# Kernel tuning notes

Hardware: AMD Instinct MI355X
Metric: run time of the kernel (lower is better)

## Reference

```python
import jax, jax.numpy as jnp
import numpy as np

N_CLASS = 50257
EMB = 1024
HID = 1024
BATCH = 1024  # must equal HID due to the module's [H,H] zero state init
SEQ = 128


def setup_inputs() -> dict:
    key = jax.random.key(0)
    ks = jax.random.split(key, 8)
    s_e = 1.0 / np.sqrt(EMB)
    s_h = 1.0 / np.sqrt(HID)
    X = jax.random.randint(ks[0], (BATCH, SEQ), 0, N_CLASS, dtype=jnp.int32)
    C = jax.random.normal(ks[1], (N_CLASS, EMB), dtype=jnp.float32)
    # gate order along last axis: i, f, g, o (each block of size HID)
    Wx = jax.random.uniform(ks[2], (EMB, 4 * HID), jnp.float32, -s_e, s_e)
    bx = jax.random.uniform(ks[3], (4 * HID,), jnp.float32, -s_e, s_e)
    Wh = jax.random.uniform(ks[4], (HID, 4 * HID), jnp.float32, -s_h, s_h)
    bh = jax.random.uniform(ks[5], (4 * HID,), jnp.float32, -s_h, s_h)
    W_out = jax.random.uniform(ks[6], (HID, N_CLASS), jnp.float32, -s_h, s_h)
    b_out = jnp.ones((N_CLASS,), dtype=jnp.float32)  # nn.Parameter(torch.ones)
    return {"X": X, "C": C, "Wx": Wx, "bx": bx, "Wh": Wh, "bh": bh,
            "W_out": W_out, "b_out": b_out}


def _lstm_last_hidden(xs, Wx, bx, Wh, bh):
    # xs: [S, B, E]; with zero-initialized h/c of shape [H,H] and B == H,
    # the original broadcast-buggy code reduces to a standard LSTM.
    x_proj = jnp.einsum('sbe,eg->sbg', xs, Wx) + bx  # [S, B, 4H]
    B = xs.shape[1]
    H = Wh.shape[0]
    h0 = jnp.zeros((B, H), dtype=xs.dtype)
    c0 = jnp.zeros((B, H), dtype=xs.dtype)

    def step(carry, xp):
        h, c = carry
        gates = xp + h @ Wh + bh  # [B, 4H]
        i, f, g, o = jnp.split(gates, 4, axis=-1)
        i = jax.nn.sigmoid(i)
        f = jax.nn.sigmoid(f)
        g = jnp.tanh(g)
        o = jax.nn.sigmoid(o)
        c = f * c + i * g
        h = o * jnp.tanh(c)
        return (h, c), None

    (h, _), _ = jax.lax.scan(step, (h0, c0), x_proj)
    return h  # [B, H] last timestep hidden


def reference(X, C, Wx, bx, Wh, bh, W_out, b_out):
    emb = C[X]                      # [B, S, E]
    xs = jnp.swapaxes(emb, 0, 1)    # [S, B, E]  (transpose(0,1))
    h_last = _lstm_last_hidden(xs, Wx, bx, Wh, bh)
    return h_last @ W_out + b_out   # [B, n_class]
```

## Files before the change

kernel.cpp:

```cpp
#include <hip/hip_runtime.h>
#include <hip/hip_bf16.h>

#define SEQ_   128
#define NCLS_  50257
#define EMB_   1024
#define HID_   1024
#define BATCH_ 1024
#define G4_    4096

typedef __attribute__((ext_vector_type(8))) short short8;
typedef __attribute__((ext_vector_type(4))) float f32x4;

__device__ __forceinline__ void async_copy16(void* lds, const void* g) {
  __builtin_amdgcn_global_load_lds(
      (const __attribute__((address_space(1))) void*)g,
      (__attribute__((address_space(3))) void*)lds, 16, 0, 0);
}

__device__ __forceinline__ void mfma_acc(f32x4& c, const short8& a, const short8& b) {
  asm("v_mfma_f32_16x16x32_bf16 %0, %1, %2, %0" : "+v"(c) : "v"(a), "v"(b));
}

__device__ __forceinline__ float sigmoidf_(float x) {
  return 1.f / (1.f + __expf(-x));
}
__device__ __forceinline__ float tanhf_(float x) {
  x = fminf(12.f, fmaxf(-12.f, x));
  float e = __expf(2.f * x);
  return (e - 1.f) / (e + 1.f);
}
__device__ __forceinline__ float bf2f_(ushort u) {
  return __uint_as_float(((unsigned int)u) << 16);
}

template <int EPI>
__global__ __launch_bounds__(256) void gemm_bt(
    const __hip_bfloat16* __restrict__ A, const __hip_bfloat16* __restrict__ Bt,
    float* __restrict__ outF, __hip_bfloat16* __restrict__ outB,
    int Mreal, int Nreal, int K, long ostride,
    const float* __restrict__ bias0) {
  __shared__ __align__(16) char smem[65536];

  const int tid = threadIdx.x;
  const int lane = tid & 63;
  const int w = tid >> 6;
  const int wm = w >> 1;
  const int wn = w & 1;
  const int m0 = blockIdx.y * 128;
  const int n0 = blockIdx.x * 128;

  const int fr = lane & 15;
  const int kb = (lane >> 4) * 16;
  const int swz = (fr & 7) << 4;

  f32x4 acc[4][4];
#pragma unroll
  for (int i = 0; i < 4; ++i)
#pragma unroll
    for (int j = 0; j < 4; ++j) acc[i][j] = (f32x4)(0.0f);

  auto STAGE = [&](int kc, int b) {
#pragma unroll
    for (int q = 0; q < 8; ++q) {
      const int ridx = (q & 3) * 256 + tid;
      const int row = ridx >> 3;
      const int ch = ridx & 7;
      const __hip_bfloat16* src;
      char* dst;
      if (q < 4) {
        long ar = m0 + row; if (ar >= Mreal) ar = Mreal - 1;
        src = A + ar * (long)K + kc * 64 + ch * 8;
        dst = smem + b * 16384 + ridx * 16;
      } else {
        long br = n0 + row; if (br >= Nreal) br = Nreal - 1;
        src = Bt + br * (long)K + kc * 64 + ch * 8;
        dst = smem + 32768 + b * 16384 + ridx * 16;
      }
      async_copy16(dst, src);
    }
  };

  const int KC = K >> 6;
  STAGE(0, 0);
  for (int kc = 0; kc < KC; ++kc) {
    const int b = kc & 1;
    if (kc + 1 < KC) {
      STAGE(kc + 1, b ^ 1);
      asm volatile("s_waitcnt vmcnt(8)" ::: "memory");
    } else {
      asm volatile("s_waitcnt vmcnt(0)" ::: "memory");
    }
    __builtin_amdgcn_s_barrier();
    __builtin_amdgcn_sched_barrier(0);

    short8 aR[2][4], bR[2][4];
#pragma unroll
    for (int kk = 0; kk < 2; ++kk)
#pragma unroll
      for (int f = 0; f < 4; ++f) {
        aR[kk][f] = *(const short8*)(smem + b * 16384 +
                     (wm * 64 + f * 16 + fr) * 128 + ((kk * 64 + kb) ^ swz));
        bR[kk][f] = *(const short8*)(smem + 32768 + b * 16384 +
                     (wn * 64 + f * 16 + fr) * 128 + ((kk * 64 + kb) ^ swz));
      }
#pragma unroll
    for (int fm = 0; fm < 4; ++fm)
#pragma unroll
      for (int fn = 0; fn < 4; ++fn) {
        mfma_acc(acc[fm][fn], aR[0][fm], bR[0][fn]);
        mfma_acc(acc[fm][fn], aR[1][fm], bR[1][fn]);
      }
    __builtin_amdgcn_sched_barrier(0);
    __builtin_amdgcn_s_barrier();
  }

  const int cn = lane & 15;
  const int rb = (lane >> 4) * 4;
#pragma unroll
  for (int fn = 0; fn < 4; ++fn) {
    const int col = n0 + wn * 64 + fn * 16 + cn;
    const float badd = (col < Nreal) ? bias0[col] : 0.f;
#pragma unroll
    for (int fm = 0; fm < 4; ++fm) {
#pragma unroll
      for (int r = 0; r < 4; ++r) {
        const int row = m0 + wm * 64 + fm * 16 + rb + r;
        const float v = acc[fm][fn][r] + badd;
        if (EPI == 0) {
          if (row < Mreal) outB[(long)row * ostride + col] = __float2bfloat16(v);
        } else {
          if (col < Nreal && row < Mreal) outF[(long)row * ostride + col] = v;
        }
      }
    }
  }
}

__global__ __launch_bounds__(256) void pack_b(const float* __restrict__ Wh,
                                              __hip_bfloat16* __restrict__ Bpk) {
  const int gtid = blockIdx.x * 256 + threadIdx.x;
  const int l = gtid & 63;
  const int tile = gtid >> 6;
  const int g = tile & 3;
  const int kk = (tile >> 2) & 1;
  const int kc = (tile >> 3) & 7;
  const int kh = (tile >> 6) & 1;
  const int wn = (tile >> 7) & 1;
  const int ht = tile >> 8;
  const int h = ht * 32 + wn * 16 + (l & 15);
  const int k0 = kh * 512 + kc * 64 + kk * 32 + (l >> 4) * 8;
  short8 v;
#pragma unroll
  for (int e = 0; e < 8; ++e) {
    const __hip_bfloat16 b = __float2bfloat16(Wh[(size_t)(k0 + e) * G4_ + g * 1024 + h]);
    v[e] = *reinterpret_cast<const short*>(&b);
  }
  *(short8*)(Bpk + (size_t)gtid * 8) = v;
}

__global__ __launch_bounds__(512, 2) void lstm_step(
    const __hip_bfloat16* __restrict__ hprev,
    const __hip_bfloat16* __restrict__ Bpk,
    const __hip_bfloat16* __restrict__ Epr,
    const int* __restrict__ X,
    float* __restrict__ cbuf,
    __hip_bfloat16* __restrict__ hnext,
    __hip_bfloat16* __restrict__ hfin,
    int t, int last) {
  extern __shared__ __align__(16) char smem[];
  float* gacc = (float*)smem;

  const int tid = threadIdx.x;
  const int lane = tid & 63;
  const int w = tid >> 6;
  const int wm = (w >> 1) & 1;
  const int wn = w & 1;
  const int kh = w >> 2;
  const int bid = blockIdx.x;
  const int xcd = bid & 7;
  const int j = bid >> 3;
  const int ht = xcd * 4 + (j & 3);
  const int mt = j >> 2;
  const int m0 = mt * 128;
  const int h0 = ht * 32;

  const int fr = lane & 15;
  const int kb = (lane >> 4) * 16;
  const int swz = (fr & 7) << 4;
  const int cn = lane & 15;
  const int rb = (lane >> 4) * 4;

  const int crow = tid >> 2;
  const int hq = tid & 3;
  const int prow = m0 + crow;
  const int tok1 = X[prow * SEQ_ + t];

  const __hip_bfloat16* bb =
      Bpk + (size_t)(((ht * 2 + wn) * 2 + kh) * 64) * 512 + lane * 8;

  f32x4 acc[4][4];
#pragma unroll
  for (int i = 0; i < 4; ++i)
#pragma unroll
    for (int g = 0; g < 4; ++g) acc[i][g] = (f32x4)(0.0f);

  auto STAGE_A = [&](int kc, int b) {
#pragma unroll
    for (int q = 0; q < 4; ++q) {
      const int region = q >> 1;
      const int r = (q & 1) * 512 + tid;
      const int row = r >> 3, ch = r & 7;
      const __hip_bfloat16* src =
          hprev + (size_t)(m0 + row) * HID_ + region * 512 + kc * 64 + ch * 8;
      async_copy16(smem + b * 32768 + region * 16384 + r * 16, src);
    }
  };

  short8 bR[2][2][4];

  STAGE_A(0, 0);
#pragma unroll
  for (int kk = 0; kk < 2; ++kk)
#pragma unroll
    for (int g = 0; g < 4; ++g)
      bR[0][kk][g] = *(const short8*)(bb + (0 * 8 + kk * 4 + g) * 512);
  STAGE_A(1, 1);

#pragma unroll
  for (int kc = 0; kc < 8; ++kc) {
    __builtin_amdgcn_s_barrier();
    if (kc + 1 < 8) {
#pragma unroll
      for (int kk = 0; kk < 2; ++kk)
#pragma unroll
        for (int g = 0; g < 4; ++g)
          bR[(kc + 1) & 1][kk][g] =
              *(const short8*)(bb + ((kc + 1) * 8 + kk * 4 + g) * 512);
    }
    if (kc + 2 < 8) STAGE_A(kc + 2, (kc + 2) % 3);
    if (kc < 6)      asm volatile("s_waitcnt vmcnt(24)" ::: "memory");
    else if (kc == 6) asm volatile("s_waitcnt vmcnt(20)" ::: "memory");
    else             asm volatile("s_waitcnt vmcnt(8)" ::: "memory");
    __builtin_amdgcn_sched_barrier(0);

    const char* baseA = smem + (kc % 3) * 32768 + kh * 16384;
    short8 aR[2][4];
#pragma unroll
    for (int kk = 0; kk < 2; ++kk)
#pragma unroll
      for (int f = 0; f < 4; ++f)
        aR[kk][f] = *(const short8*)(baseA + (wm * 64 + f * 16 + fr) * 128 +
                                     ((kk * 64 + kb) ^ swz));
    __builtin_amdgcn_s_setprio(1);
#pragma unroll
    for (int fm = 0; fm < 4; ++fm)
#pragma unroll
      for (int g = 0; g < 4; ++g) {
        mfma_acc(acc[fm][g], aR[0][fm], bR[kc & 1][0][g]);
        mfma_acc(acc[fm][g], aR[1][fm], bR[kc & 1][1][g]);
      }
    __builtin_amdgcn_s_setprio(0);
  }

  ushort4 ep[8];
  float cold[8];
#pragma unroll
  for (int jj = 0; jj < 8; ++jj) {
    ep[jj] = *(const ushort4*)(Epr + (size_t)tok1 * G4_ + (h0 + hq * 8 + jj) * 4);
    cold[jj] = cbuf[(size_t)prow * HID_ + h0 + hq * 8 + jj];
  }

  __syncthreads();
  if (kh == 0) {
#pragma unroll
    for (int fm = 0; fm < 4; ++fm)
#pragma unroll
      for (int g = 0; g < 4; ++g)
#pragma unroll
        for (int r = 0; r < 4; ++r)
          gacc[(wm * 64 + fm * 16 + rb + r) * 132 + (wn * 16 + cn) * 4 + g] =
              acc[fm][g][r];
  }
  __syncthreads();
  if (kh == 1) {
#pragma unroll
    for (int fm = 0; fm < 4; ++fm)
#pragma unroll
      for (int g = 0; g < 4; ++g)
#pragma unroll
        for (int r = 0; r < 4; ++r)
          gacc[(wm * 64 + fm * 16 + rb + r) * 132 + (wn * 16 + cn) * 4 + g] +=
              acc[fm][g][r];
  }
  __syncthreads();

  const float* gr = gacc + crow * 132 + hq * 32;
  f32x4 cnew0, cnew1;
  short8 hv;
#pragma unroll
  for (int jj = 0; jj < 8; ++jj) {
    const f32x4 g4 = *(const f32x4*)(gr + jj * 4);
    const float iv = sigmoidf_(g4[0] + bf2f_(ep[jj].x));
    const float fv = sigmoidf_(g4[1] + bf2f_(ep[jj].y));
    const float gv = tanhf_(g4[2] + bf2f_(ep[jj].z));
    const float ov = sigmoidf_(g4[3] + bf2f_(ep[jj].w));
    const float cv = fv * cold[jj] + iv * gv;
    if (jj < 4) cnew0[jj] = cv; else cnew1[jj - 4] = cv;
    const float hval = ov * tanhf_(cv);
    const __hip_bfloat16 hb = __float2bfloat16(hval);
    hv[jj] = *reinterpret_cast<const short*>(&hb);
  }
  float* cdst = cbuf + (size_t)prow * HID_ + h0 + hq * 8;
  *(f32x4*)cdst = cnew0;
  *(f32x4*)(cdst + 4) = cnew1;
  const int hcolb = h0 + hq * 8;
  const int hswb = (hcolb & ~63) | ((hcolb & 63) ^ ((prow & 7) << 3));
  *(short8*)(hnext + (size_t)prow * HID_ + hswb) = hv;
  if (last) *(short8*)(hfin + (size_t)prow * HID_ + hswb) = hv;
}

template <bool SWZ>
__global__ __launch_bounds__(256) void conv_bf16_k(const float* __restrict__ in,
                                                   __hip_bfloat16* __restrict__ out, int n4) {
  const int i = blockIdx.x * 256 + threadIdx.x;
  if (i >= n4) return;
  const float4 v = ((const float4*)in)[i];
  int o = i * 4;
  if (SWZ) {
    const int row = o >> 10, col = o & 1023;
    const int cs = (col & ~63) | ((col & 63) ^ ((row & 7) << 3));
    o = (o & ~1023) | cs;
  }
  out[o + 0] = __float2bfloat16(v.x);
  out[o + 1] = __float2bfloat16(v.y);
  out[o + 2] = __float2bfloat16(v.z);
  out[o + 3] = __float2bfloat16(v.w);
}

template <bool PERM, bool SWZ>
__global__ __launch_bounds__(256) void transpose_conv(const float* __restrict__ in,
                                                      __hip_bfloat16* __restrict__ out,
                                                      int R, int C) {
  __shared__ float tile[32][33];
  const int c0 = blockIdx.x * 32, r0 = blockIdx.y * 32;
  const int tx = threadIdx.x, ty = threadIdx.y;
#pragma unroll
  for (int i = 0; i < 4; ++i) {
    const int r = r0 + ty + i * 8, cc = c0 + tx;
    tile[ty + i * 8][tx] = (r < R && cc < C) ? in[(size_t)r * C + cc] : 0.f;
  }
  __syncthreads();
#pragma unroll
  for (int i = 0; i < 4; ++i) {
    const int ro = c0 + ty + i * 8, co = r0 + tx;
    if (ro < C && co < R) {
      const int n = PERM ? ((ro & 1023) * 4 + (ro >> 10)) : ro;
      int k = co;
      if (SWZ) k = (k & ~63) | ((k & 63) ^ ((n & 7) << 3));
      out[(size_t)n * R + k] = __float2bfloat16(tile[tx][ty + i * 8]);
    }
  }
}

__global__ __launch_bounds__(256) void bias_perm(const float* __restrict__ bx,
                                                 const float* __restrict__ bh,
                                                 float* __restrict__ bP) {
  const int n = blockIdx.x * 256 + threadIdx.x;
  if (n >= G4_) return;
  const int h = n >> 2, g = n & 3;
  bP[n] = bx[g * HID_ + h] + bh[g * HID_ + h];
}

extern "C" void kernel_launch(void* const* d_in, const int* in_sizes, int n_in,
                              void* d_out, int out_size, void* d_ws, size_t ws_size,
                              hipStream_t stream) {
  const int* X = (const int*)d_in[0];
  const float* C = (const float*)d_in[1];
  const float* Wx = (const float*)d_in[2];
  const float* bx = (const float*)d_in[3];
  const float* Wh = (const float*)d_in[4];
  const float* bh = (const float*)d_in[5];
  const float* Wo = (const float*)d_in[6];
  const float* bo = (const float*)d_in[7];
  float* out = (float*)d_out;

  char* p = (char*)d_ws;
  const size_t szCb  = (size_t)NCLS_ * EMB_ * 2;
  const size_t szWxt = (size_t)G4_ * EMB_ * 2;
  const size_t szBpk = (size_t)G4_ * HID_ * 2;
  const size_t szEpr = (size_t)NCLS_ * G4_ * 2;
  const size_t szH   = (size_t)BATCH_ * HID_ * 2;
  const size_t szC   = (size_t)BATCH_ * HID_ * 4;
  const size_t szBp  = (size_t)G4_ * 4;
  if (ws_size < szCb + szWxt + szBpk + szEpr + 3 * szH + szC + szBp) return;

  __hip_bfloat16* Cb   = (__hip_bfloat16*)p; p += szCb;
  __hip_bfloat16* WxtP = (__hip_bfloat16*)p; p += szWxt;
  __hip_bfloat16* Bpk  = (__hip_bfloat16*)p; p += szBpk;
  __hip_bfloat16* Epr  = (__hip_bfloat16*)p; p += szEpr;
  __hip_bfloat16* hA   = (__hip_bfloat16*)p; p += szH;
  __hip_bfloat16* hB   = (__hip_bfloat16*)p; p += szH;
  __hip_bfloat16* hfin = (__hip_bfloat16*)p; p += szH;
  float* cbuf          = (float*)p;          p += szC;
  float* bP            = (float*)p;          p += szBp;

  {
    const int n4 = NCLS_ * EMB_ / 4;
    conv_bf16_k<true><<<(n4 + 255) / 256, 256, 0, stream>>>(C, Cb, n4);
  }
  transpose_conv<true, true><<<dim3(G4_ / 32, EMB_ / 32), dim3(32, 8), 0, stream>>>(
      Wx, WxtP, EMB_, G4_);
  pack_b<<<2048, 256, 0, stream>>>(Wh, Bpk);
  bias_perm<<<G4_ / 256, 256, 0, stream>>>(bx, bh, bP);

  gemm_bt<0><<<dim3(G4_ / 128, (NCLS_ + 127) / 128), 256, 0, stream>>>(
      Cb, WxtP, nullptr, Epr, NCLS_, G4_, EMB_, G4_, bP);

  hipMemsetAsync(hA, 0, szH, stream);
  hipMemsetAsync(cbuf, 0, szC, stream);

  for (int t = 0; t < SEQ_; ++t) {
    const __hip_bfloat16* hp = (t & 1) ? hB : hA;
    __hip_bfloat16* hn = (t & 1) ? hA : hB;
    lstm_step<<<256, 512, 98304, stream>>>(hp, Bpk, Epr, X, cbuf, hn, hfin, t,
                                           (int)(t == SEQ_ - 1));
  }

  __hip_bfloat16* Wot = Cb;
  transpose_conv<false, true><<<dim3((NCLS_ + 31) / 32, HID_ / 32), dim3(32, 8), 0,
                                stream>>>(Wo, Wot, HID_, NCLS_);

  gemm_bt<2><<<dim3((NCLS_ + 127) / 128, BATCH_ / 128), 256, 0, stream>>>(
      hfin, Wot, out, nullptr, BATCH_, NCLS_, HID_, NCLS_, bo);
}
```

Measured before the change: 3.162 ms.

## Halve LSTM step tile to 16 hidden units, 256 threads, 512 blocks

Each recurrent step block now covers 128 rows by 16 hidden units (all four gates interleaved in the packed Wh layout) with 4 waves instead of 8, and the grid doubles to 512 blocks. The A-operand pipeline drops from triple to double buffering with a static 64KB LDS footprint, and a second barrier is added per k-chunk. The aim is more blocks per CU and better latency hiding with a smaller LDS footprint. The trade-off is that each block now re-reads the full hprev rows for half as much output, doubling A traffic, and adds extra synchronisation.

```diff
diff --git a/kernel.cpp b/kernel.cpp
--- a/kernel.cpp
+++ b/kernel.cpp
@@ -141,13 +141,14 @@
   const int gtid = blockIdx.x * 256 + threadIdx.x;
   const int l = gtid & 63;
   const int tile = gtid >> 6;
-  const int g = tile & 3;
+  const int j = tile & 3;
   const int kk = (tile >> 2) & 1;
   const int kc = (tile >> 3) & 7;
   const int kh = (tile >> 6) & 1;
-  const int wn = (tile >> 7) & 1;
-  const int ht = tile >> 8;
-  const int h = ht * 32 + wn * 16 + (l & 15);
+  const int ht = tile >> 7;
+  const int c = l & 15;
+  const int h = ht * 16 + j * 4 + (c >> 2);
+  const int g = c & 3;
   const int k0 = kh * 512 + kc * 64 + kk * 32 + (l >> 4) * 8;
   short8 v;
 #pragma unroll
@@ -158,7 +159,7 @@
   *(short8*)(Bpk + (size_t)gtid * 8) = v;
 }
 
-__global__ __launch_bounds__(512, 2) void lstm_step(
+__global__ __launch_bounds__(256, 2) void lstm_step(
     const __hip_bfloat16* __restrict__ hprev,
     const __hip_bfloat16* __restrict__ Bpk,
     const __hip_bfloat16* __restrict__ Epr,
@@ -167,22 +168,21 @@
     __hip_bfloat16* __restrict__ hnext,
     __hip_bfloat16* __restrict__ hfin,
     int t, int last) {
-  extern __shared__ __align__(16) char smem[];
+  __shared__ __align__(16) char smem[65536];
   float* gacc = (float*)smem;
 
   const int tid = threadIdx.x;
   const int lane = tid & 63;
   const int w = tid >> 6;
-  const int wm = (w >> 1) & 1;
-  const int wn = w & 1;
-  const int kh = w >> 2;
+  const int wm = w & 1;
+  const int kh = w >> 1;
   const int bid = blockIdx.x;
   const int xcd = bid & 7;
-  const int j = bid >> 3;
-  const int ht = xcd * 4 + (j & 3);
-  const int mt = j >> 2;
+  const int r9 = bid >> 3;
+  const int ht = xcd * 8 + (r9 & 7);
+  const int mt = r9 >> 3;
   const int m0 = mt * 128;
-  const int h0 = ht * 32;
+  const int h0 = ht * 16;
 
   const int fr = lane & 15;
   const int kb = (lane >> 4) * 16;
@@ -190,25 +190,24 @@
   const int cn = lane & 15;
   const int rb = (lane >> 4) * 4;
 
-  const int crow = tid >> 2;
-  const int hq = tid & 3;
+  const int crow = tid >> 1;
+  const int hh = (tid & 1) * 8;
   const int prow = m0 + crow;
   const int tok1 = X[prow * SEQ_ + t];
 
-  const __hip_bfloat16* bb =
-      Bpk + (size_t)(((ht * 2 + wn) * 2 + kh) * 64) * 512 + lane * 8;
+  const __hip_bfloat16* bb = Bpk + (size_t)((ht * 2 + kh) * 64) * 512 + lane * 8;
 
   f32x4 acc[4][4];
 #pragma unroll
   for (int i = 0; i < 4; ++i)
 #pragma unroll
-    for (int g = 0; g < 4; ++g) acc[i][g] = (f32x4)(0.0f);
+    for (int jj = 0; jj < 4; ++jj) acc[i][jj] = (f32x4)(0.0f);
 
   auto STAGE_A = [&](int kc, int b) {
 #pragma unroll
-    for (int q = 0; q < 4; ++q) {
-      const int region = q >> 1;
-      const int r = (q & 1) * 512 + tid;
+    for (int q = 0; q < 8; ++q) {
+      const int region = q >> 2;
+      const int r = (q & 3) * 256 + tid;
       const int row = r >> 3, ch = r & 7;
       const __hip_bfloat16* src =
           hprev + (size_t)(m0 + row) * HID_ + region * 512 + kc * 64 + ch * 8;
@@ -217,33 +216,29 @@
   };
 
   short8 bR[2][2][4];
+  auto LOAD_B = [&](int kc) {
+#pragma unroll
+    for (int kk = 0; kk < 2; ++kk)
+#pragma unroll
+      for (int jj = 0; jj < 4; ++jj)
+        bR[kc & 1][kk][jj] = *(const short8*)(bb + (kc * 8 + kk * 4 + jj) * 512);
+  };
 
   STAGE_A(0, 0);
-#pragma unroll
-  for (int kk = 0; kk < 2; ++kk)
-#pragma unroll
-    for (int g = 0; g < 4; ++g)
-      bR[0][kk][g] = *(const short8*)(bb + (0 * 8 + kk * 4 + g) * 512);
-  STAGE_A(1, 1);
-
-#pragma unroll
+  LOAD_B(0);
   for (int kc = 0; kc < 8; ++kc) {
+    const int b = kc & 1;
+    if (kc + 1 < 8) {
+      STAGE_A(kc + 1, b ^ 1);
+      LOAD_B(kc + 1);
+      asm volatile("s_waitcnt vmcnt(16)" ::: "memory");
+    } else {
+      asm volatile("s_waitcnt vmcnt(0)" ::: "memory");
+    }
     __builtin_amdgcn_s_barrier();
-    if (kc + 1 < 8) {
-#pragma unroll
-      for (int kk = 0; kk < 2; ++kk)
-#pragma unroll
-        for (int g = 0; g < 4; ++g)
-          bR[(kc + 1) & 1][kk][g] =
-              *(const short8*)(bb + ((kc + 1) * 8 + kk * 4 + g) * 512);
-    }
-    if (kc + 2 < 8) STAGE_A(kc + 2, (kc + 2) % 3);
-    if (kc < 6)      asm volatile("s_waitcnt vmcnt(24)" ::: "memory");
-    else if (kc == 6) asm volatile("s_waitcnt vmcnt(20)" ::: "memory");
-    else             asm volatile("s_waitcnt vmcnt(8)" ::: "memory");
     __builtin_amdgcn_sched_barrier(0);
 
-    const char* baseA = smem + (kc % 3) * 32768 + kh * 16384;
+    const char* baseA = smem + b * 32768 + kh * 16384;
     short8 aR[2][4];
 #pragma unroll
     for (int kk = 0; kk < 2; ++kk)
@@ -255,19 +250,21 @@
 #pragma unroll
     for (int fm = 0; fm < 4; ++fm)
 #pragma unroll
-      for (int g = 0; g < 4; ++g) {
-        mfma_acc(acc[fm][g], aR[0][fm], bR[kc & 1][0][g]);
-        mfma_acc(acc[fm][g], aR[1][fm], bR[kc & 1][1][g]);
+      for (int jj = 0; jj < 4; ++jj) {
+        mfma_acc(acc[fm][jj], aR[0][fm], bR[b][0][jj]);
+        mfma_acc(acc[fm][jj], aR[1][fm], bR[b][1][jj]);
       }
     __builtin_amdgcn_s_setprio(0);
+    __builtin_amdgcn_sched_barrier(0);
+    __builtin_amdgcn_s_barrier();
   }
 
   ushort4 ep[8];
   float cold[8];
 #pragma unroll
   for (int jj = 0; jj < 8; ++jj) {
-    ep[jj] = *(const ushort4*)(Epr + (size_t)tok1 * G4_ + (h0 + hq * 8 + jj) * 4);
-    cold[jj] = cbuf[(size_t)prow * HID_ + h0 + hq * 8 + jj];
+    ep[jj] = *(const ushort4*)(Epr + (size_t)tok1 * G4_ + (h0 + hh + jj) * 4);
+    cold[jj] = cbuf[(size_t)prow * HID_ + h0 + hh + jj];
   }
 
   __syncthreads();
@@ -275,26 +272,24 @@
 #pragma unroll
     for (int fm = 0; fm < 4; ++fm)
 #pragma unroll
-      for (int g = 0; g < 4; ++g)
+      for (int jj = 0; jj < 4; ++jj)
 #pragma unroll
         for (int r = 0; r < 4; ++r)
-          gacc[(wm * 64 + fm * 16 + rb + r) * 132 + (wn * 16 + cn) * 4 + g] =
-              acc[fm][g][r];
+          gacc[(wm * 64 + fm * 16 + rb + r) * 68 + jj * 16 + cn] = acc[fm][jj][r];
   }
   __syncthreads();
   if (kh == 1) {
 #pragma unroll
     for (int fm = 0; fm < 4; ++fm)
 #pragma unroll
-      for (int g = 0; g < 4; ++g)
+      for (int jj = 0; jj < 4; ++jj)
 #pragma unroll
         for (int r = 0; r < 4; ++r)
-          gacc[(wm * 64 + fm * 16 + rb + r) * 132 + (wn * 16 + cn) * 4 + g] +=
-              acc[fm][g][r];
+          gacc[(wm * 64 + fm * 16 + rb + r) * 68 + jj * 16 + cn] += acc[fm][jj][r];
   }
   __syncthreads();
 
-  const float* gr = gacc + crow * 132 + hq * 32;
+  const float* gr = gacc + crow * 68 + hh * 4;
   f32x4 cnew0, cnew1;
   short8 hv;
 #pragma unroll
@@ -310,10 +305,10 @@
     const __hip_bfloat16 hb = __float2bfloat16(hval);
     hv[jj] = *reinterpret_cast<const short*>(&hb);
   }
-  float* cdst = cbuf + (size_t)prow * HID_ + h0 + hq * 8;
+  float* cdst = cbuf + (size_t)prow * HID_ + h0 + hh;
   *(f32x4*)cdst = cnew0;
   *(f32x4*)(cdst + 4) = cnew1;
-  const int hcolb = h0 + hq * 8;
+  const int hcolb = h0 + hh;
   const int hswb = (hcolb & ~63) | ((hcolb & 63) ^ ((prow & 7) << 3));
   *(short8*)(hnext + (size_t)prow * HID_ + hswb) = hv;
   if (last) *(short8*)(hfin + (size_t)prow * HID_ + hswb) = hv;
@@ -422,8 +417,8 @@
   for (int t = 0; t < SEQ_; ++t) {
     const __hip_bfloat16* hp = (t & 1) ? hB : hA;
     __hip_bfloat16* hn = (t & 1) ? hA : hB;
-    lstm_step<<<256, 512, 98304, stream>>>(hp, Bpk, Epr, X, cbuf, hn, hfin, t,
-                                           (int)(t == SEQ_ - 1));
+    lstm_step<<<512, 256, 0, stream>>>(hp, Bpk, Epr, X, cbuf, hn, hfin, t,
+                                       (int)(t == SEQ_ - 1));
   }
 
   __hip_bfloat16* Wot = Cb;
```

Result: slower. 3.305 ms (+4.5%).

## Replace GEMMs with 128x256 tile kernel loading prepacked B fragments directly to registers

Applied to the files above, without the earlier changes.

Replaces the 128x128 LDS-staged GEMM with a 512-thread, 128x256-tile kernel. Only A is staged through LDS, using a 3-slot async pipeline. B (Wx and W_out) is prepacked into MFMA-fragment order so each wave loads its fragments straight from global memory into double-buffered registers. New pack_wx/pack_wo kernels replace the transpose kernels, and block indices are remapped for locality. This cuts LDS traffic and barriers per MFMA, but costs more registers and extra packing passes with strided reads.

```diff
diff --git a/kernel.cpp b/kernel.cpp
--- a/kernel.cpp
+++ b/kernel.cpp
@@ -34,106 +34,178 @@
 }
 
 template <int EPI>
-__global__ __launch_bounds__(256) void gemm_bt(
-    const __hip_bfloat16* __restrict__ A, const __hip_bfloat16* __restrict__ Bt,
+__global__ __launch_bounds__(512) void gemm256(
+    const __hip_bfloat16* __restrict__ A,
+    const __hip_bfloat16* __restrict__ Bpk,
     float* __restrict__ outF, __hip_bfloat16* __restrict__ outB,
-    int Mreal, int Nreal, int K, long ostride,
-    const float* __restrict__ bias0) {
-  __shared__ __align__(16) char smem[65536];
+    int Mreal, int Nreal, long ostride, const float* __restrict__ bias0) {
+  __shared__ __align__(16) __hip_bfloat16 lA[3 * 128 * 64];
 
   const int tid = threadIdx.x;
   const int lane = tid & 63;
   const int w = tid >> 6;
-  const int wm = w >> 1;
-  const int wn = w & 1;
-  const int m0 = blockIdx.y * 128;
-  const int n0 = blockIdx.x * 128;
+  const int wm = w >> 2;
+  const int wn = w & 3;
+
+  int tx, ty;
+  if constexpr (EPI == 0) {
+    const int om = blockIdx.x & 7;
+    const int idx = blockIdx.x >> 3;
+    tx = om * 2 + (idx & 1);
+    ty = idx >> 1;
+  } else {
+    tx = blockIdx.x >> 3;
+    ty = blockIdx.x & 7;
+  }
+  const int m0 = ty * 128;
+  const int n0 = tx * 256;
 
   const int fr = lane & 15;
   const int kb = (lane >> 4) * 16;
   const int swz = (fr & 7) << 4;
 
+  const __hip_bfloat16* bb = Bpk + (size_t)(tx * 4 + wn) * 128 * 512 + lane * 8;
+
   f32x4 acc[4][4];
 #pragma unroll
   for (int i = 0; i < 4; ++i)
 #pragma unroll
     for (int j = 0; j < 4; ++j) acc[i][j] = (f32x4)(0.0f);
 
-  auto STAGE = [&](int kc, int b) {
-#pragma unroll
-    for (int q = 0; q < 8; ++q) {
-      const int ridx = (q & 3) * 256 + tid;
-      const int row = ridx >> 3;
-      const int ch = ridx & 7;
-      const __hip_bfloat16* src;
-      char* dst;
-      if (q < 4) {
-        long ar = m0 + row; if (ar >= Mreal) ar = Mreal - 1;
-        src = A + ar * (long)K + kc * 64 + ch * 8;
-        dst = smem + b * 16384 + ridx * 16;
-      } else {
-        long br = n0 + row; if (br >= Nreal) br = Nreal - 1;
-        src = Bt + br * (long)K + kc * 64 + ch * 8;
-        dst = smem + 32768 + b * 16384 + ridx * 16;
-      }
-      async_copy16(dst, src);
+  auto STAGE = [&](int kc, int slot) {
+#pragma unroll
+    for (int q = 0; q < 2; ++q) {
+      const int r = q * 512 + tid;
+      const int row = r >> 3, ch = r & 7;
+      long ar = m0 + row;
+      if (EPI == 0 && ar >= Mreal) ar = Mreal - 1;
+      async_copy16((char*)lA + slot * 16384 + r * 16,
+                   (const char*)(A + ar * 1024 + kc * 64 + ch * 8));
     }
   };
 
-  const int KC = K >> 6;
+  short8 bR[2][2][4];
+  auto LOADB = [&](int kc) {
+#pragma unroll
+    for (int kk = 0; kk < 2; ++kk)
+#pragma unroll
+      for (int nf = 0; nf < 4; ++nf)
+        bR[kc & 1][kk][nf] =
+            *(const short8*)(bb + (nf * 32 + kc * 2 + kk) * 512);
+  };
+
+  LOADB(0);
+  __builtin_amdgcn_sched_barrier(0);
   STAGE(0, 0);
-  for (int kc = 0; kc < KC; ++kc) {
-    const int b = kc & 1;
-    if (kc + 1 < KC) {
-      STAGE(kc + 1, b ^ 1);
-      asm volatile("s_waitcnt vmcnt(8)" ::: "memory");
-    } else {
-      asm volatile("s_waitcnt vmcnt(0)" ::: "memory");
-    }
-    __builtin_amdgcn_s_barrier();
+  STAGE(1, 1);
+  __builtin_amdgcn_sched_barrier(0);
+  asm volatile("s_waitcnt vmcnt(2)" ::: "memory");
+  __builtin_amdgcn_s_barrier();
+
+#pragma unroll 2
+  for (int kc = 0; kc < 16; ++kc) {
+    if (kc < 15) LOADB(kc + 1);
     __builtin_amdgcn_sched_barrier(0);
-
-    short8 aR[2][4], bR[2][4];
-#pragma unroll
-    for (int kk = 0; kk < 2; ++kk)
-#pragma unroll
-      for (int f = 0; f < 4; ++f) {
-        aR[kk][f] = *(const short8*)(smem + b * 16384 +
-                     (wm * 64 + f * 16 + fr) * 128 + ((kk * 64 + kb) ^ swz));
-        bR[kk][f] = *(const short8*)(smem + 32768 + b * 16384 +
-                     (wn * 64 + f * 16 + fr) * 128 + ((kk * 64 + kb) ^ swz));
-      }
+    if (kc < 14) STAGE(kc + 2, (kc + 2) % 3);
+    __builtin_amdgcn_sched_barrier(0);
+
+    const char* baseA = (const char*)lA + (kc % 3) * 16384;
+    short8 aR[4];
+#pragma unroll
+    for (int f = 0; f < 4; ++f)
+      aR[f] = *(const short8*)(baseA + (wm * 64 + f * 16 + fr) * 128 +
+                               (kb ^ swz));
+    __builtin_amdgcn_s_setprio(1);
 #pragma unroll
     for (int fm = 0; fm < 4; ++fm)
 #pragma unroll
-      for (int fn = 0; fn < 4; ++fn) {
-        mfma_acc(acc[fm][fn], aR[0][fm], bR[0][fn]);
-        mfma_acc(acc[fm][fn], aR[1][fm], bR[1][fn]);
-      }
+      for (int nf = 0; nf < 4; ++nf)
+        mfma_acc(acc[fm][nf], aR[fm], bR[kc & 1][0][nf]);
+    __builtin_amdgcn_s_setprio(0);
+#pragma unroll
+    for (int f = 0; f < 4; ++f)
+      aR[f] = *(const short8*)(baseA + (wm * 64 + f * 16 + fr) * 128 +
+                               ((64 + kb) ^ swz));
+    __builtin_amdgcn_s_setprio(1);
+#pragma unroll
+    for (int fm = 0; fm < 4; ++fm)
+#pragma unroll
+      for (int nf = 0; nf < 4; ++nf)
+        mfma_acc(acc[fm][nf], aR[fm], bR[kc & 1][1][nf]);
+    __builtin_amdgcn_s_setprio(0);
     __builtin_amdgcn_sched_barrier(0);
-    __builtin_amdgcn_s_barrier();
+
+    if (kc < 14)       asm volatile("s_waitcnt vmcnt(2)" ::: "memory");
+    else if (kc == 14) asm volatile("s_waitcnt vmcnt(0)" ::: "memory");
+    if (kc < 15) __builtin_amdgcn_s_barrier();
   }
 
   const int cn = lane & 15;
   const int rb = (lane >> 4) * 4;
 #pragma unroll
-  for (int fn = 0; fn < 4; ++fn) {
-    const int col = n0 + wn * 64 + fn * 16 + cn;
-    const float badd = (col < Nreal) ? bias0[col] : 0.f;
+  for (int nf = 0; nf < 4; ++nf) {
+    const int col = n0 + wn * 64 + nf * 16 + cn;
+    const float badd = (EPI == 0) ? bias0[col]
+                                  : ((col < Nreal) ? bias0[col] : 0.f);
 #pragma unroll
     for (int fm = 0; fm < 4; ++fm) {
 #pragma unroll
       for (int r = 0; r < 4; ++r) {
         const int row = m0 + wm * 64 + fm * 16 + rb + r;
-        const float v = acc[fm][fn][r] + badd;
+        const float v = acc[fm][nf][r] + badd;
         if (EPI == 0) {
           if (row < Mreal) outB[(long)row * ostride + col] = __float2bfloat16(v);
         } else {
-          if (col < Nreal && row < Mreal) outF[(long)row * ostride + col] = v;
+          if (col < Nreal) outF[(long)row * ostride + col] = v;
         }
       }
     }
   }
+}
+
+__global__ __launch_bounds__(256) void pack_wx(const float* __restrict__ Wx,
+                                               __hip_bfloat16* __restrict__ Bpk) {
+  const int gtid = blockIdx.x * 256 + threadIdx.x;
+  const int l = gtid & 63;
+  const int tile = gtid >> 6;
+  const int kk = tile & 1;
+  const int kc = (tile >> 1) & 15;
+  const int nf = (tile >> 5) & 3;
+  const int wn = (tile >> 7) & 3;
+  const int tx = tile >> 9;
+  const int n = tx * 256 + wn * 64 + nf * 16 + (l & 15);
+  const int g = n & 3, h = n >> 2;
+  const int k0 = kc * 64 + kk * 32 + (l >> 4) * 8;
+  short8 v;
+#pragma unroll
+  for (int e = 0; e < 8; ++e) {
+    const __hip_bfloat16 b =
+        __float2bfloat16(Wx[(size_t)(k0 + e) * G4_ + g * 1024 + h]);
+    v[e] = *reinterpret_cast<const short*>(&b);
+  }
+  *(short8*)(Bpk + (size_t)gtid * 8) = v;
+}
+
+__global__ __launch_bounds__(256) void pack_wo(const float* __restrict__ Wo,
+                                               __hip_bfloat16* __restrict__ Bpk) {
+  const int gtid = blockIdx.x * 256 + threadIdx.x;
+  const int l = gtid & 63;
+  const int tile = gtid >> 6;
+  const int kk = tile & 1;
+  const int kc = (tile >> 1) & 15;
+  const int nf = (tile >> 5) & 3;
+  const int wn = (tile >> 7) & 3;
+  const int tx = tile >> 9;
+  const int n = tx * 256 + wn * 64 + nf * 16 + (l & 15);
+  const int k0 = kc * 64 + kk * 32 + (l >> 4) * 8;
+  short8 v;
+#pragma unroll
+  for (int e = 0; e < 8; ++e) {
+    float f = (n < NCLS_) ? Wo[(size_t)(k0 + e) * NCLS_ + n] : 0.f;
+    const __hip_bfloat16 b = __float2bfloat16(f);
+    v[e] = *reinterpret_cast<const short*>(&b);
+  }
+  *(short8*)(Bpk + (size_t)gtid * 8) = v;
 }
 
 __global__ __launch_bounds__(256) void pack_b(const float* __restrict__ Wh,
@@ -337,31 +409,6 @@
   out[o + 3] = __float2bfloat16(v.w);
 }
 
-template <bool PERM, bool SWZ>
-__global__ __launch_bounds__(256) void transpose_conv(const float* __restrict__ in,
-                                                      __hip_bfloat16* __restrict__ out,
-                                                      int R, int C) {
-  __shared__ float tile[32][33];
-  const int c0 = blockIdx.x * 32, r0 = blockIdx.y * 32;
-  const int tx = threadIdx.x, ty = threadIdx.y;
-#pragma unroll
-  for (int i = 0; i < 4; ++i) {
-    const int r = r0 + ty + i * 8, cc = c0 + tx;
-    tile[ty + i * 8][tx] = (r < R && cc < C) ? in[(size_t)r * C + cc] : 0.f;
-  }
-  __syncthreads();
-#pragma unroll
-  for (int i = 0; i < 4; ++i) {
-    const int ro = c0 + ty + i * 8, co = r0 + tx;
-    if (ro < C && co < R) {
-      const int n = PERM ? ((ro & 1023) * 4 + (ro >> 10)) : ro;
-      int k = co;
-      if (SWZ) k = (k & ~63) | ((k & 63) ^ ((n & 7) << 3));
-      out[(size_t)n * R + k] = __float2bfloat16(tile[tx][ty + i * 8]);
-    }
-  }
-}
-
 __global__ __launch_bounds__(256) void bias_perm(const float* __restrict__ bx,
                                                  const float* __restrict__ bh,
                                                  float* __restrict__ bP) {
@@ -385,17 +432,20 @@
   float* out = (float*)d_out;
 
   char* p = (char*)d_ws;
-  const size_t szCb  = (size_t)NCLS_ * EMB_ * 2;
-  const size_t szWxt = (size_t)G4_ * EMB_ * 2;
-  const size_t szBpk = (size_t)G4_ * HID_ * 2;
-  const size_t szEpr = (size_t)NCLS_ * G4_ * 2;
-  const size_t szH   = (size_t)BATCH_ * HID_ * 2;
-  const size_t szC   = (size_t)BATCH_ * HID_ * 4;
-  const size_t szBp  = (size_t)G4_ * 4;
-  if (ws_size < szCb + szWxt + szBpk + szEpr + 3 * szH + szC + szBp) return;
-
-  __hip_bfloat16* Cb   = (__hip_bfloat16*)p; p += szCb;
-  __hip_bfloat16* WxtP = (__hip_bfloat16*)p; p += szWxt;
+  const size_t szCb   = (size_t)NCLS_ * EMB_ * 2;
+  const size_t szPad  = (size_t)G4_ * EMB_ * 2;
+  const size_t szBpk2 = (size_t)G4_ * HID_ * 2;
+  const size_t szBpk  = (size_t)G4_ * HID_ * 2;
+  const size_t szEpr  = (size_t)NCLS_ * G4_ * 2;
+  const size_t szH    = (size_t)BATCH_ * HID_ * 2;
+  const size_t szC    = (size_t)BATCH_ * HID_ * 4;
+  const size_t szBp   = (size_t)G4_ * 4;
+  if (ws_size < szCb + szPad + szBpk2 + szBpk + szEpr + 3 * szH + szC + szBp)
+    return;
+
+  __hip_bfloat16* Cb   = (__hip_bfloat16*)p;
+  __hip_bfloat16* Wopk = (__hip_bfloat16*)p; p += szCb + szPad;
+  __hip_bfloat16* Bpk2 = (__hip_bfloat16*)p; p += szBpk2;
   __hip_bfloat16* Bpk  = (__hip_bfloat16*)p; p += szBpk;
   __hip_bfloat16* Epr  = (__hip_bfloat16*)p; p += szEpr;
   __hip_bfloat16* hA   = (__hip_bfloat16*)p; p += szH;
@@ -408,13 +458,14 @@
     const int n4 = NCLS_ * EMB_ / 4;
     conv_bf16_k<true><<<(n4 + 255) / 256, 256, 0, stream>>>(C, Cb, n4);
   }
-  transpose_conv<true, true><<<dim3(G4_ / 32, EMB_ / 32), dim3(32, 8), 0, stream>>>(
-      Wx, WxtP, EMB_, G4_);
+  pack_wx<<<2048, 256, 0, stream>>>(Wx, Bpk2);
   pack_b<<<2048, 256, 0, stream>>>(Wh, Bpk);
   bias_perm<<<G4_ / 256, 256, 0, stream>>>(bx, bh, bP);
 
-  gemm_bt<0><<<dim3(G4_ / 128, (NCLS_ + 127) / 128), 256, 0, stream>>>(
-      Cb, WxtP, nullptr, Epr, NCLS_, G4_, EMB_, G4_, bP);
+  gemm256<0><<<dim3(6304), 512, 0, stream>>>(
+      Cb, Bpk2, nullptr, Epr, NCLS_, G4_, G4_, bP);
+
+  pack_wo<<<25216, 256, 0, stream>>>(Wo, Wopk);
 
   hipMemsetAsync(hA, 0, szH, stream);
   hipMemsetAsync(cbuf, 0, szC, stream);
@@ -426,10 +477,6 @@
                                            (int)(t == SEQ_ - 1));
   }
 
-  __hip_bfloat16* Wot = Cb;
-  transpose_conv<false, true><<<dim3((NCLS_ + 31) / 32, HID_ / 32), dim3(32, 8), 0,
-                                stream>>>(Wo, Wot, HID_, NCLS_);
-
-  gemm_bt<2><<<dim3((NCLS_ + 127) / 128, BATCH_ / 128), 256, 0, stream>>>(
-      hfin, Wot, out, nullptr, BATCH_, NCLS_, HID_, NCLS_, bo);
-}
+  gemm256<2><<<dim3(1576), 512, 0, stream>>>(
+      hfin, Wopk, out, nullptr, BATCH_, NCLS_, NCLS_, bo);
+}
```

New measurement: 3.458 ms. 9.4% more time.

## Replace GEMM with 8-wave 128x256 tile, triple-buffered LDS pipeline

Applied to the files above, without the earlier changes.

The shared bf16 GEMM used for the vocabulary-wide input projection and the output projection now uses 512 threads, a 128x256 output tile, and a three-stage LDS ring in dynamic shared memory (147 KB). Global-to-LDS loads for the tile two steps ahead are issued in halves between MFMA phases, and s_setprio raises wave priority around the MFMA blocks. This aims to hide load latency better and raise compute per staged byte, at the cost of more LDS, which limits occupancy to one block per CU. K is now hardcoded to 1024.

```diff
diff --git a/kernel.cpp b/kernel.cpp
--- a/kernel.cpp
+++ b/kernel.cpp
@@ -34,20 +34,20 @@
 }
 
 template <int EPI>
-__global__ __launch_bounds__(256) void gemm_bt(
-    const __hip_bfloat16* __restrict__ A, const __hip_bfloat16* __restrict__ Bt,
+__global__ __launch_bounds__(512) void gemm8p(
+    const __hip_bfloat16* __restrict__ A,
+    const __hip_bfloat16* __restrict__ Bt,
     float* __restrict__ outF, __hip_bfloat16* __restrict__ outB,
-    int Mreal, int Nreal, int K, long ostride,
-    const float* __restrict__ bias0) {
-  __shared__ __align__(16) char smem[65536];
+    int Mreal, int Nreal, long ostride, const float* __restrict__ bias0) {
+  extern __shared__ __align__(16) char smem[];
 
   const int tid = threadIdx.x;
   const int lane = tid & 63;
   const int w = tid >> 6;
-  const int wm = w >> 1;
-  const int wn = w & 1;
+  const int wm = w >> 2;
+  const int wn = w & 3;
   const int m0 = blockIdx.y * 128;
-  const int n0 = blockIdx.x * 128;
+  const int n0 = blockIdx.x * 256;
 
   const int fr = lane & 15;
   const int kb = (lane >> 4) * 16;
@@ -59,59 +59,68 @@
 #pragma unroll
     for (int j = 0; j < 4; ++j) acc[i][j] = (f32x4)(0.0f);
 
-  auto STAGE = [&](int kc, int b) {
-#pragma unroll
-    for (int q = 0; q < 8; ++q) {
-      const int ridx = (q & 3) * 256 + tid;
-      const int row = ridx >> 3;
-      const int ch = ridx & 7;
+  auto STAGE3 = [&](int kc, int part) {
+    const int slot = kc % 3;
+#pragma unroll
+    for (int q = 0; q < 3; ++q) {
+      const int inst = part * 3 + q;
+      char* dst;
       const __hip_bfloat16* src;
-      char* dst;
-      if (q < 4) {
+      if (inst < 2) {
+        const int r = inst * 512 + tid;
+        const int row = r >> 3, ch = r & 7;
         long ar = m0 + row; if (ar >= Mreal) ar = Mreal - 1;
-        src = A + ar * (long)K + kc * 64 + ch * 8;
-        dst = smem + b * 16384 + ridx * 16;
+        src = A + ar * 1024 + kc * 64 + ch * 8;
+        dst = smem + slot * 49152 + r * 16;
       } else {
+        const int r = (inst - 2) * 512 + tid;
+        const int row = r >> 3, ch = r & 7;
         long br = n0 + row; if (br >= Nreal) br = Nreal - 1;
-        src = Bt + br * (long)K + kc * 64 + ch * 8;
-        dst = smem + 32768 + b * 16384 + ridx * 16;
+        src = Bt + br * 1024 + kc * 64 + ch * 8;
+        dst = smem + slot * 49152 + 16384 + r * 16;
       }
       async_copy16(dst, src);
     }
   };
 
-  const int KC = K >> 6;
-  STAGE(0, 0);
-  for (int kc = 0; kc < KC; ++kc) {
-    const int b = kc & 1;
-    if (kc + 1 < KC) {
-      STAGE(kc + 1, b ^ 1);
-      asm volatile("s_waitcnt vmcnt(8)" ::: "memory");
-    } else {
-      asm volatile("s_waitcnt vmcnt(0)" ::: "memory");
-    }
-    __builtin_amdgcn_s_barrier();
-    __builtin_amdgcn_sched_barrier(0);
-
-    short8 aR[2][4], bR[2][4];
-#pragma unroll
-    for (int kk = 0; kk < 2; ++kk)
+  STAGE3(0, 0); STAGE3(0, 1);
+  STAGE3(1, 0); STAGE3(1, 1);
+  asm volatile("s_waitcnt vmcnt(6)" ::: "memory");
+  __builtin_amdgcn_s_barrier();
+
+  for (int t = 0; t < 16; ++t) {
+    const char* baseA = smem + (t % 3) * 49152;
+    const char* baseB = baseA + 16384;
+#pragma unroll
+    for (int kk = 0; kk < 2; ++kk) {
+      if (t + 2 < 16) STAGE3(t + 2, kk);
+      __builtin_amdgcn_sched_barrier(0);
+
+      short8 aR[4], bR[4];
 #pragma unroll
       for (int f = 0; f < 4; ++f) {
-        aR[kk][f] = *(const short8*)(smem + b * 16384 +
-                     (wm * 64 + f * 16 + fr) * 128 + ((kk * 64 + kb) ^ swz));
-        bR[kk][f] = *(const short8*)(smem + 32768 + b * 16384 +
-                     (wn * 64 + f * 16 + fr) * 128 + ((kk * 64 + kb) ^ swz));
+        aR[f] = *(const short8*)(baseA + (wm * 64 + f * 16 + fr) * 128 +
+                                 ((kk * 64 + kb) ^ swz));
+        bR[f] = *(const short8*)(baseB + (wn * 64 + f * 16 + fr) * 128 +
+                                 ((kk * 64 + kb) ^ swz));
       }
-#pragma unroll
-    for (int fm = 0; fm < 4; ++fm)
-#pragma unroll
-      for (int fn = 0; fn < 4; ++fn) {
-        mfma_acc(acc[fm][fn], aR[0][fm], bR[0][fn]);
-        mfma_acc(acc[fm][fn], aR[1][fm], bR[1][fn]);
+      __builtin_amdgcn_s_barrier();
+      asm volatile("s_waitcnt lgkmcnt(0)" ::: "memory");
+      __builtin_amdgcn_sched_barrier(0);
+      __builtin_amdgcn_s_setprio(1);
+#pragma unroll
+      for (int fm = 0; fm < 4; ++fm)
+#pragma unroll
+        for (int fn = 0; fn < 4; ++fn)
+          mfma_acc(acc[fm][fn], aR[fm], bR[fn]);
+      __builtin_amdgcn_s_setprio(0);
+      __builtin_amdgcn_sched_barrier(0);
+      if (kk == 1) {
+        if (t < 14)       asm volatile("s_waitcnt vmcnt(6)" ::: "memory");
+        else if (t == 14) asm volatile("s_waitcnt vmcnt(0)" ::: "memory");
       }
-    __builtin_amdgcn_sched_barrier(0);
-    __builtin_amdgcn_s_barrier();
+      __builtin_amdgcn_s_barrier();
+    }
   }
 
   const int cn = lane & 15;
@@ -119,7 +128,8 @@
 #pragma unroll
   for (int fn = 0; fn < 4; ++fn) {
     const int col = n0 + wn * 64 + fn * 16 + cn;
-    const float badd = (col < Nreal) ? bias0[col] : 0.f;
+    const float badd = (EPI == 0) ? bias0[col]
+                                  : ((col < Nreal) ? bias0[col] : 0.f);
 #pragma unroll
     for (int fm = 0; fm < 4; ++fm) {
 #pragma unroll
@@ -129,7 +139,7 @@
         if (EPI == 0) {
           if (row < Mreal) outB[(long)row * ostride + col] = __float2bfloat16(v);
         } else {
-          if (col < Nreal && row < Mreal) outF[(long)row * ostride + col] = v;
+          if (col < Nreal) outF[(long)row * ostride + col] = v;
         }
       }
     }
@@ -413,8 +423,8 @@
   pack_b<<<2048, 256, 0, stream>>>(Wh, Bpk);
   bias_perm<<<G4_ / 256, 256, 0, stream>>>(bx, bh, bP);
 
-  gemm_bt<0><<<dim3(G4_ / 128, (NCLS_ + 127) / 128), 256, 0, stream>>>(
-      Cb, WxtP, nullptr, Epr, NCLS_, G4_, EMB_, G4_, bP);
+  gemm8p<0><<<dim3(G4_ / 256, (NCLS_ + 127) / 128), 512, 147456, stream>>>(
+      Cb, WxtP, nullptr, Epr, NCLS_, G4_, G4_, bP);
 
   hipMemsetAsync(hA, 0, szH, stream);
   hipMemsetAsync(cbuf, 0, szC, stream);
@@ -430,6 +440,6 @@
   transpose_conv<false, true><<<dim3((NCLS_ + 31) / 32, HID_ / 32), dim3(32, 8), 0,
                                 stream>>>(Wo, Wot, HID_, NCLS_);
 
-  gemm_bt<2><<<dim3((NCLS_ + 127) / 128, BATCH_ / 128), 256, 0, stream>>>(
-      hfin, Wot, out, nullptr, BATCH_, NCLS_, HID_, NCLS_, bo);
-}
+  gemm8p<2><<<dim3((NCLS_ + 255) / 256, BATCH_ / 128), 512, 147456, stream>>>(
+      hfin, Wot, out, nullptr, BATCH_, NCLS_, NCLS_, bo);
+}
```

New measurement: 3.168 ms. About the same (+0.2%).
